# Kernel optimization log

Hardware: AMD Instinct MI355X
Metric: run time of the kernel (lower is better)

The kernel has to match this reference:

```python
import jax, jax.numpy as jnp
import numpy as np

B, H, S, D = 4, 16, 4096, 64

def setup_inputs() -> dict:
    key = jax.random.key(0)
    k1, k2, k3 = jax.random.split(key, 3)
    Q = jax.random.normal(k1, (B, H, S, D), dtype=jnp.float32)
    K = jax.random.normal(k2, (B, H, S, D), dtype=jnp.float32)
    V = jax.random.normal(k3, (B, H, S, D), dtype=jnp.float32)
    mask = jnp.ones((B, H, S), dtype=jnp.float32)
    return {"Q": Q, "K": K, "V": V, "mask": mask}

def reference(Q, K, V, mask):
    # elu(x)+1 feature map
    Qf = jax.nn.elu(Q) + 1.0
    Kf = (jax.nn.elu(K) + 1.0) * mask[..., None]
    # KV: [B,H,D,D] = sum_s K[s]^T V[s]
    KV = jnp.einsum('bhsd,bhse->bhde', Kf, V)
    # normalization: Z = 1 / (Q . sum_s K[s])  -> [B,H,S,1]
    Ksum = jnp.sum(Kf, axis=-2)  # [B,H,D]
    Z = 1.0 / jnp.einsum('bhsd,bhd->bhs', Qf, Ksum)[..., None]
    out = jnp.einsum('bhsd,bhde->bhse', Qf, KV) * Z
    return out
```

## Files before the change

kernel.cpp:

```cpp
#include <hip/hip_runtime.h>

#define S_LEN 4096
#define DIM 64
#define NHEAD 64
#define PHEAD 4160
#define LDR 68

__device__ __forceinline__ float elu1(float x) {
    return x > 0.0f ? x + 1.0f : __expf(x);
}

__global__ __launch_bounds__(256, 4) void pass1_kv(
    const float* __restrict__ K, const float* __restrict__ V,
    const float* __restrict__ mask, float* __restrict__ partials, int sh)
{
    const int head = blockIdx.x >> sh;
    const int blkc = blockIdx.x & ((1 << sh) - 1);
    const int t    = threadIdx.x;
    const int lane = t & 63;
    const int wave = t >> 6;
    const int ex   = lane & 7;
    const int dy   = lane >> 3;
    const int e0   = ex * 8;
    const int d0   = dy * 8;

    const int rows_per_wave = (S_LEN >> sh) >> 2;
    const int ntiles = rows_per_wave >> 3;
    const int srow0  = (blkc * 4 + wave) * rows_per_wave;

    __shared__ float sm[4][2][2][8 * LDR];

    const long hbase = (long)head * S_LEN * DIM;

    float acc[8][8];
    #pragma unroll
    for (int i = 0; i < 8; ++i)
        #pragma unroll
        for (int j = 0; j < 8; ++j) acc[i][j] = 0.f;
    float ks[8] = {0.f,0.f,0.f,0.f,0.f,0.f,0.f,0.f};

    float4 kr[2], vr[2];
    float  mr[2];
    auto load_tile = [&](int tile) {
        const int srow = srow0 + tile * 8;
        #pragma unroll
        for (int j = 0; j < 2; ++j) {
            const int v4   = j * 64 + lane;
            const int row  = v4 >> 4;
            const int colg = (v4 & 15) * 4;
            kr[j] = *(const float4*)(K + hbase + (long)(srow + row) * DIM + colg);
            vr[j] = *(const float4*)(V + hbase + (long)(srow + row) * DIM + colg);
            mr[j] = mask[head * S_LEN + srow + row];
        }
    };

    load_tile(0);
    for (int tile = 0; tile < ntiles; ++tile) {
        float* kf = sm[wave][tile & 1][0];
        float* vf = sm[wave][tile & 1][1];
        #pragma unroll
        for (int j = 0; j < 2; ++j) {
            const int v4   = j * 64 + lane;
            const int row  = v4 >> 4;
            const int colg = (v4 & 15) * 4;
            float4 ko;
            ko.x = elu1(kr[j].x) * mr[j]; ko.y = elu1(kr[j].y) * mr[j];
            ko.z = elu1(kr[j].z) * mr[j]; ko.w = elu1(kr[j].w) * mr[j];
            *(float4*)&kf[row * LDR + colg] = ko;
            *(float4*)&vf[row * LDR + colg] = vr[j];
        }
        if (tile + 1 < ntiles) load_tile(tile + 1);
        __builtin_amdgcn_wave_barrier();
        #pragma unroll 2
        for (int s = 0; s < 8; ++s) {
            float kk[8], vv[8];
            *(float4*)&kk[0] = *(const float4*)&kf[s * LDR + d0];
            *(float4*)&kk[4] = *(const float4*)&kf[s * LDR + d0 + 4];
            *(float4*)&vv[0] = *(const float4*)&vf[s * LDR + e0];
            *(float4*)&vv[4] = *(const float4*)&vf[s * LDR + e0 + 4];
            #pragma unroll
            for (int ei = 0; ei < 8; ++ei)
                #pragma unroll
                for (int di = 0; di < 8; ++di)
                    acc[ei][di] += kk[di] * vv[ei];
            #pragma unroll
            for (int di = 0; di < 8; ++di) ks[di] += kk[di];
        }
        __builtin_amdgcn_wave_barrier();
    }

    __syncthreads();
    float* red = (float*)sm;
    for (int w = 0; w < 4; ++w) {
        if (wave == w) {
            if (w == 0) {
                #pragma unroll
                for (int ei = 0; ei < 8; ++ei) {
                    *(float4*)&red[(e0 + ei) * 64 + d0]     = make_float4(acc[ei][0], acc[ei][1], acc[ei][2], acc[ei][3]);
                    *(float4*)&red[(e0 + ei) * 64 + d0 + 4] = make_float4(acc[ei][4], acc[ei][5], acc[ei][6], acc[ei][7]);
                }
                if (ex == 0) {
                    *(float4*)&red[4096 + d0]     = make_float4(ks[0], ks[1], ks[2], ks[3]);
                    *(float4*)&red[4096 + d0 + 4] = make_float4(ks[4], ks[5], ks[6], ks[7]);
                }
            } else {
                #pragma unroll
                for (int ei = 0; ei < 8; ++ei) {
                    float4 a = *(float4*)&red[(e0 + ei) * 64 + d0];
                    a.x += acc[ei][0]; a.y += acc[ei][1]; a.z += acc[ei][2]; a.w += acc[ei][3];
                    *(float4*)&red[(e0 + ei) * 64 + d0] = a;
                    float4 b = *(float4*)&red[(e0 + ei) * 64 + d0 + 4];
                    b.x += acc[ei][4]; b.y += acc[ei][5]; b.z += acc[ei][6]; b.w += acc[ei][7];
                    *(float4*)&red[(e0 + ei) * 64 + d0 + 4] = b;
                }
                if (ex == 0) {
                    float4 a = *(float4*)&red[4096 + d0];
                    a.x += ks[0]; a.y += ks[1]; a.z += ks[2]; a.w += ks[3];
                    *(float4*)&red[4096 + d0] = a;
                    float4 b = *(float4*)&red[4096 + d0 + 4];
                    b.x += ks[4]; b.y += ks[5]; b.z += ks[6]; b.w += ks[7];
                    *(float4*)&red[4096 + d0 + 4] = b;
                }
            }
        }
        __syncthreads();
    }
    float* P = partials + (long)((head << sh) + blkc) * PHEAD;
    for (int i = t; i < PHEAD / 4; i += 256)
        *(float4*)(P + i * 4) = *(const float4*)&red[i * 4];
}

__global__ __launch_bounds__(256) void reduce_kv(
    const float* __restrict__ partials, float* __restrict__ kvf, int nchunk)
{
    const int head  = blockIdx.x >> 3;
    const int slice = blockIdx.x & 7;
    const int lo = slice * (PHEAD / 8);
    const int hi = lo + (PHEAD / 8);
    for (int idx = lo + threadIdx.x; idx < hi; idx += 256) {
        float s = 0.f;
        for (int c = 0; c < nchunk; ++c)
            s += partials[((long)head * nchunk + c) * PHEAD + idx];
        kvf[(long)head * PHEAD + idx] = s;
    }
}

__global__ __launch_bounds__(256, 4) void pass2_out(
    const float* __restrict__ Q, const float* __restrict__ kvf,
    float* __restrict__ out)
{
    const int head = blockIdx.x >> 4;
    const int tile = blockIdx.x & 15;
    const int t    = threadIdx.x;
    const int lane = t & 63;
    const int wave = t >> 6;

    __shared__ float sm[4][64 * 36];
    float* sl = sm[wave];

    const long hbase = (long)head * S_LEN * DIM;
    const int  rbase = tile * 256 + wave * 64;

    float q[64];
    #pragma unroll
    for (int h = 0; h < 2; ++h) {
        #pragma unroll
        for (int i = 0; i < 8; ++i) {
            const int v4  = i * 64 + lane;
            const int row = v4 >> 3;
            const int g   = v4 & 7;
            const float4 qv = *(const float4*)(Q + hbase + (long)(rbase + row) * DIM + h * 32 + g * 4);
            float4 qo;
            qo.x = elu1(qv.x); qo.y = elu1(qv.y); qo.z = elu1(qv.z); qo.w = elu1(qv.w);
            *(float4*)&sl[row * 36 + ((g + row) & 7) * 4] = qo;
        }
        __builtin_amdgcn_wave_barrier();
        #pragma unroll
        for (int g = 0; g < 8; ++g) {
            const float4 v = *(const float4*)&sl[lane * 36 + ((g + lane) & 7) * 4];
            q[h * 32 + g * 4 + 0] = v.x; q[h * 32 + g * 4 + 1] = v.y;
            q[h * 32 + g * 4 + 2] = v.z; q[h * 32 + g * 4 + 3] = v.w;
        }
        __builtin_amdgcn_wave_barrier();
    }

    const float* __restrict__ kvt = kvf + (long)head * PHEAD;

    float denom = 0.f;
    #pragma unroll
    for (int d = 0; d < 64; ++d) denom += q[d] * kvt[64 * 64 + d];
    const float rz = 1.0f / denom;

    #pragma unroll
    for (int h = 0; h < 2; ++h) {
        #pragma unroll 1
        for (int eg = 0; eg < 8; ++eg) {
            const float* __restrict__ r = kvt + (h * 8 + eg) * 256;
            float a[4];
            #pragma unroll
            for (int er = 0; er < 4; ++er) {
                float s = 0.f;
                #pragma unroll
                for (int d = 0; d < 64; ++d) s += q[d] * r[er * 64 + d];
                a[er] = s;
            }
            *(float4*)&sl[lane * 36 + ((eg + lane) & 7) * 4] =
                make_float4(a[0] * rz, a[1] * rz, a[2] * rz, a[3] * rz);
        }
        __builtin_amdgcn_wave_barrier();
        #pragma unroll
        for (int i = 0; i < 8; ++i) {
            const int v4  = i * 64 + lane;
            const int row = v4 >> 3;
            const int g   = v4 & 7;
            const float4 o = *(const float4*)&sl[row * 36 + ((g + row) & 7) * 4];
            *(float4*)(out + hbase + (long)(rbase + row) * DIM + h * 32 + g * 4) = o;
        }
        __builtin_amdgcn_wave_barrier();
    }
}

extern "C" void kernel_launch(void* const* d_in, const int* in_sizes, int n_in,
                              void* d_out, int out_size, void* d_ws, size_t ws_size,
                              hipStream_t stream) {
    const float* Q    = (const float*)d_in[0];
    const float* K    = (const float*)d_in[1];
    const float* V    = (const float*)d_in[2];
    const float* mask = (const float*)d_in[3];
    float* out = (float*)d_out;

    const size_t need16 = ((size_t)NHEAD * 16 * PHEAD + (size_t)NHEAD * PHEAD) * sizeof(float);
    const int sh = (ws_size >= need16) ? 4 : 3;
    const int nchunk = 1 << sh;

    float* partials = (float*)d_ws;
    float* kvf = partials + (size_t)NHEAD * nchunk * PHEAD;

    pass1_kv<<<NHEAD * nchunk, 256, 0, stream>>>(K, V, mask, partials, sh);
    reduce_kv<<<NHEAD * 8, 256, 0, stream>>>(partials, kvf, nchunk);
    pass2_out<<<NHEAD * 16, 256, 0, stream>>>(Q, kvf, out);
}
```

Measured before the change: 315.4 us.

## Restructure work split: 512-thread KV blocks, column-split output rows across waves

Pass 1 now uses 512-thread blocks with eight waves over fixed 8 chunks per head, dropping the double-buffered per-wave LDS tiles. Pass 2 now has each block handle 64 rows with all four waves sharing the same rows, each computing a quarter of the output columns, using XOR-swizzled shared tiles and block barriers. The intent is less per-wave redundant KV streaming in pass 2, more blocks, and a simpler reduction path. The trade-off is an extra block-wide sync, more serialized LDS reduction steps in pass 1, and the loss of double buffering.

```diff
diff --git a/kernel.cpp b/kernel.cpp
--- a/kernel.cpp
+++ b/kernel.cpp
@@ -3,6 +3,7 @@
 #define S_LEN 4096
 #define DIM 64
 #define NHEAD 64
+#define NCHUNK 8
 #define PHEAD 4160
 #define LDR 68
 
@@ -10,12 +11,12 @@
     return x > 0.0f ? x + 1.0f : __expf(x);
 }
 
-__global__ __launch_bounds__(256, 4) void pass1_kv(
+__global__ __launch_bounds__(512, 4) void pass1_kv(
     const float* __restrict__ K, const float* __restrict__ V,
-    const float* __restrict__ mask, float* __restrict__ partials, int sh)
+    const float* __restrict__ mask, float* __restrict__ partials)
 {
-    const int head = blockIdx.x >> sh;
-    const int blkc = blockIdx.x & ((1 << sh) - 1);
+    const int head = blockIdx.x >> 3;
+    const int blkc = blockIdx.x & 7;
     const int t    = threadIdx.x;
     const int lane = t & 63;
     const int wave = t >> 6;
@@ -24,11 +25,9 @@
     const int e0   = ex * 8;
     const int d0   = dy * 8;
 
-    const int rows_per_wave = (S_LEN >> sh) >> 2;
-    const int ntiles = rows_per_wave >> 3;
-    const int srow0  = (blkc * 4 + wave) * rows_per_wave;
-
-    __shared__ float sm[4][2][2][8 * LDR];
+    const int srow0 = blkc * 512 + wave * 64;
+
+    __shared__ float sm[8][2][8 * LDR];
 
     const long hbase = (long)head * S_LEN * DIM;
 
@@ -54,10 +53,11 @@
         }
     };
 
+    float* kf = sm[wave][0];
+    float* vf = sm[wave][1];
+
     load_tile(0);
-    for (int tile = 0; tile < ntiles; ++tile) {
-        float* kf = sm[wave][tile & 1][0];
-        float* vf = sm[wave][tile & 1][1];
+    for (int tile = 0; tile < 8; ++tile) {
         #pragma unroll
         for (int j = 0; j < 2; ++j) {
             const int v4   = j * 64 + lane;
@@ -69,7 +69,7 @@
             *(float4*)&kf[row * LDR + colg] = ko;
             *(float4*)&vf[row * LDR + colg] = vr[j];
         }
-        if (tile + 1 < ntiles) load_tile(tile + 1);
+        if (tile + 1 < 8) load_tile(tile + 1);
         __builtin_amdgcn_wave_barrier();
         #pragma unroll 2
         for (int s = 0; s < 8; ++s) {
@@ -91,7 +91,7 @@
 
     __syncthreads();
     float* red = (float*)sm;
-    for (int w = 0; w < 4; ++w) {
+    for (int w = 0; w < 8; ++w) {
         if (wave == w) {
             if (w == 0) {
                 #pragma unroll
@@ -125,13 +125,13 @@
         }
         __syncthreads();
     }
-    float* P = partials + (long)((head << sh) + blkc) * PHEAD;
-    for (int i = t; i < PHEAD / 4; i += 256)
+    float* P = partials + (long)(head * NCHUNK + blkc) * PHEAD;
+    for (int i = t; i < PHEAD / 4; i += 512)
         *(float4*)(P + i * 4) = *(const float4*)&red[i * 4];
 }
 
 __global__ __launch_bounds__(256) void reduce_kv(
-    const float* __restrict__ partials, float* __restrict__ kvf, int nchunk)
+    const float* __restrict__ partials, float* __restrict__ kvf)
 {
     const int head  = blockIdx.x >> 3;
     const int slice = blockIdx.x & 7;
@@ -139,8 +139,9 @@
     const int hi = lo + (PHEAD / 8);
     for (int idx = lo + threadIdx.x; idx < hi; idx += 256) {
         float s = 0.f;
-        for (int c = 0; c < nchunk; ++c)
-            s += partials[((long)head * nchunk + c) * PHEAD + idx];
+        #pragma unroll
+        for (int c = 0; c < NCHUNK; ++c)
+            s += partials[((long)head * NCHUNK + c) * PHEAD + idx];
         kvf[(long)head * PHEAD + idx] = s;
     }
 }
@@ -149,39 +150,35 @@
     const float* __restrict__ Q, const float* __restrict__ kvf,
     float* __restrict__ out)
 {
-    const int head = blockIdx.x >> 4;
-    const int tile = blockIdx.x & 15;
+    const int head = blockIdx.x >> 6;
+    const int tile = blockIdx.x & 63;
     const int t    = threadIdx.x;
     const int lane = t & 63;
     const int wave = t >> 6;
 
-    __shared__ float sm[4][64 * 36];
-    float* sl = sm[wave];
+    __shared__ float q_sl[64 * 64];
+    __shared__ float o_sl[64 * 64];
 
     const long hbase = (long)head * S_LEN * DIM;
-    const int  rbase = tile * 256 + wave * 64;
+    const int  rbase = tile * 64;
+
+    #pragma unroll
+    for (int i = 0; i < 4; ++i) {
+        const int v4  = i * 256 + t;
+        const int row = v4 >> 4;
+        const int g   = v4 & 15;
+        const float4 qv = *(const float4*)(Q + hbase + (long)(rbase + row) * DIM + g * 4);
+        float4 qo;
+        qo.x = elu1(qv.x); qo.y = elu1(qv.y); qo.z = elu1(qv.z); qo.w = elu1(qv.w);
+        *(float4*)&q_sl[row * 64 + ((g ^ (row & 15)) * 4)] = qo;
+    }
+    __syncthreads();
 
     float q[64];
     #pragma unroll
-    for (int h = 0; h < 2; ++h) {
-        #pragma unroll
-        for (int i = 0; i < 8; ++i) {
-            const int v4  = i * 64 + lane;
-            const int row = v4 >> 3;
-            const int g   = v4 & 7;
-            const float4 qv = *(const float4*)(Q + hbase + (long)(rbase + row) * DIM + h * 32 + g * 4);
-            float4 qo;
-            qo.x = elu1(qv.x); qo.y = elu1(qv.y); qo.z = elu1(qv.z); qo.w = elu1(qv.w);
-            *(float4*)&sl[row * 36 + ((g + row) & 7) * 4] = qo;
-        }
-        __builtin_amdgcn_wave_barrier();
-        #pragma unroll
-        for (int g = 0; g < 8; ++g) {
-            const float4 v = *(const float4*)&sl[lane * 36 + ((g + lane) & 7) * 4];
-            q[h * 32 + g * 4 + 0] = v.x; q[h * 32 + g * 4 + 1] = v.y;
-            q[h * 32 + g * 4 + 2] = v.z; q[h * 32 + g * 4 + 3] = v.w;
-        }
-        __builtin_amdgcn_wave_barrier();
+    for (int g = 0; g < 16; ++g) {
+        const float4 v = *(const float4*)&q_sl[lane * 64 + ((g ^ (lane & 15)) * 4)];
+        q[g * 4 + 0] = v.x; q[g * 4 + 1] = v.y; q[g * 4 + 2] = v.z; q[g * 4 + 3] = v.w;
     }
 
     const float* __restrict__ kvt = kvf + (long)head * PHEAD;
@@ -191,32 +188,30 @@
     for (int d = 0; d < 64; ++d) denom += q[d] * kvt[64 * 64 + d];
     const float rz = 1.0f / denom;
 
-    #pragma unroll
-    for (int h = 0; h < 2; ++h) {
-        #pragma unroll 1
-        for (int eg = 0; eg < 8; ++eg) {
-            const float* __restrict__ r = kvt + (h * 8 + eg) * 256;
-            float a[4];
+    #pragma unroll 1
+    for (int j = 0; j < 4; ++j) {
+        const int cg = wave * 4 + j;
+        const float* __restrict__ r = kvt + cg * 256;
+        float a[4];
+        #pragma unroll
+        for (int er = 0; er < 4; ++er) {
+            float s = 0.f;
             #pragma unroll
-            for (int er = 0; er < 4; ++er) {
-                float s = 0.f;
-                #pragma unroll
-                for (int d = 0; d < 64; ++d) s += q[d] * r[er * 64 + d];
-                a[er] = s;
-            }
-            *(float4*)&sl[lane * 36 + ((eg + lane) & 7) * 4] =
-                make_float4(a[0] * rz, a[1] * rz, a[2] * rz, a[3] * rz);
-        }
-        __builtin_amdgcn_wave_barrier();
-        #pragma unroll
-        for (int i = 0; i < 8; ++i) {
-            const int v4  = i * 64 + lane;
-            const int row = v4 >> 3;
-            const int g   = v4 & 7;
-            const float4 o = *(const float4*)&sl[row * 36 + ((g + row) & 7) * 4];
-            *(float4*)(out + hbase + (long)(rbase + row) * DIM + h * 32 + g * 4) = o;
-        }
-        __builtin_amdgcn_wave_barrier();
+            for (int d = 0; d < 64; ++d) s += q[d] * r[er * 64 + d];
+            a[er] = s;
+        }
+        *(float4*)&o_sl[lane * 64 + ((cg ^ (lane & 15)) * 4)] =
+            make_float4(a[0] * rz, a[1] * rz, a[2] * rz, a[3] * rz);
+    }
+    __syncthreads();
+
+    #pragma unroll
+    for (int i = 0; i < 4; ++i) {
+        const int v4  = i * 256 + t;
+        const int row = v4 >> 4;
+        const int g   = v4 & 15;
+        const float4 o = *(const float4*)&o_sl[row * 64 + ((g ^ (row & 15)) * 4)];
+        *(float4*)(out + hbase + (long)(rbase + row) * DIM + g * 4) = o;
     }
 }
 
@@ -229,14 +224,10 @@
     const float* mask = (const float*)d_in[3];
     float* out = (float*)d_out;
 
-    const size_t need16 = ((size_t)NHEAD * 16 * PHEAD + (size_t)NHEAD * PHEAD) * sizeof(float);
-    const int sh = (ws_size >= need16) ? 4 : 3;
-    const int nchunk = 1 << sh;
-
     float* partials = (float*)d_ws;
-    float* kvf = partials + (size_t)NHEAD * nchunk * PHEAD;
-
-    pass1_kv<<<NHEAD * nchunk, 256, 0, stream>>>(K, V, mask, partials, sh);
-    reduce_kv<<<NHEAD * 8, 256, 0, stream>>>(partials, kvf, nchunk);
-    pass2_out<<<NHEAD * 16, 256, 0, stream>>>(Q, kvf, out);
-}
+    float* kvf = partials + (size_t)NHEAD * NCHUNK * PHEAD;
+
+    pass1_kv<<<NHEAD * NCHUNK, 512, 0, stream>>>(K, V, mask, partials);
+    reduce_kv<<<NHEAD * 8, 256, 0, stream>>>(partials, kvf);
+    pass2_out<<<NHEAD * 64, 256, 0, stream>>>(Q, kvf, out);
+}
```

Result: slower. 910.4 us (+188.7%).
